# Kernel optimization log

Measured on AMD Instinct MI355X. Metric: run time of the kernel, lower is better.

## Reference

```python
import jax, jax.numpy as jnp
import numpy as np

NORM_EPS = 1e-5
HEAD_DIM = 32
SR_RATIO = 2
N_RATIO = SR_RATIO ** 2  # avg-pool kernel/stride over sequence


def setup_inputs() -> dict:
    key = jax.random.key(0)
    ks = jax.random.split(key, 12)
    B, N, C = 4, 3136, 384
    s = 0.02
    inp = {
        "x": jax.random.normal(ks[0], (B, N, C), dtype=jnp.float32),
        "Wq": jax.random.normal(ks[1], (C, C), dtype=jnp.float32) * s,
        "bq": jnp.zeros((C,), jnp.float32),
        "Wk": jax.random.normal(ks[2], (C, C), dtype=jnp.float32) * s,
        "bk": jnp.zeros((C,), jnp.float32),
        "Wv": jax.random.normal(ks[3], (C, C), dtype=jnp.float32) * s,
        "bv": jnp.zeros((C,), jnp.float32),
        "Wp": jax.random.normal(ks[4], (C, C), dtype=jnp.float32) * s,
        "bp": jnp.zeros((C,), jnp.float32),
        "bn_gamma": jnp.ones((C,), jnp.float32),
        "bn_beta": jnp.zeros((C,), jnp.float32),
        "bn_mean": jax.random.normal(ks[5], (C,), dtype=jnp.float32) * 0.1,
        "bn_var": jax.random.uniform(ks[6], (C,), dtype=jnp.float32, minval=0.5, maxval=1.5),
    }
    return inp


def reference(x, Wq, bq, Wk, bk, Wv, bv, Wp, bp, bn_gamma, bn_beta, bn_mean, bn_var):
    B, N, C = x.shape
    H = C // HEAD_DIM
    d = HEAD_DIM
    scale = d ** -0.5

    # q projection -> [B, H, N, d]
    q = (x @ Wq.T + bq).reshape(B, N, H, d)

    # sequence reduction: AvgPool1d(kernel=stride=N_RATIO) over tokens
    Nk = N // N_RATIO
    x_ = x.reshape(B, Nk, N_RATIO, C).mean(axis=2)  # [B, Nk, C]
    # BatchNorm1d over channel dim (inference / running-stats form)
    x_ = (x_ - bn_mean) * jax.lax.rsqrt(bn_var + NORM_EPS) * bn_gamma + bn_beta

    k = (x_ @ Wk.T + bk).reshape(B, Nk, H, d)
    v = (x_ @ Wv.T + bv).reshape(B, Nk, H, d)

    attn = jnp.einsum("bnhd,bmhd->bhnm", q, k) * scale  # [B, H, N, Nk]
    attn = jax.nn.softmax(attn, axis=-1)
    out = jnp.einsum("bhnm,bmhd->bnhd", attn, v).reshape(B, N, C)
    return out @ Wp.T + bp
```

## Files before the change

### kernel.cpp

```cpp
#include <hip/hip_runtime.h>


typedef __bf16 bf16x8 __attribute__((ext_vector_type(8)));
typedef unsigned short u16x8 __attribute__((ext_vector_type(8)));
typedef float f32x4 __attribute__((ext_vector_type(4)));

#define NTOK 3136
#define NKV 784
#define CCH 384
#define KPAD 832
#define SC2 0.25503472078024693f

#define WAIT_BAR(N) asm volatile("s_waitcnt vmcnt(" #N ")\n\ts_barrier" ::: "memory")

__device__ __forceinline__ unsigned short f2b(float f) {
  union { float f; unsigned u; } v; v.f = f;
  unsigned r = v.u + 0x7fffu + ((v.u >> 16) & 1u);
  return (unsigned short)(r >> 16);
}

__device__ __forceinline__ bf16x8 ldsb8(const unsigned short* p) {
  u16x8 v = *(const u16x8*)p;
  return __builtin_bit_cast(bf16x8, v);
}

__device__ __forceinline__ void gload16(const void* g, void* lds) {
  auto* g1 = reinterpret_cast<const __attribute__((address_space(1))) unsigned int*>(
      reinterpret_cast<uintptr_t>(g));
  auto* l3 = reinterpret_cast<__attribute__((address_space(3))) unsigned int*>(
      reinterpret_cast<uintptr_t>(lds));
  __builtin_amdgcn_global_load_lds(g1, l3, 16, 0, 0);
}

__global__ __launch_bounds__(256) void prep_kernel(
    const float* __restrict__ x, const float* __restrict__ gam,
    const float* __restrict__ bet, const float* __restrict__ mea,
    const float* __restrict__ var,
    const float* __restrict__ Wq, const float* __restrict__ Wk,
    const float* __restrict__ Wv, const float* __restrict__ Wp,
    unsigned short* __restrict__ xb, unsigned short* __restrict__ xpb,
    unsigned short* __restrict__ wq, unsigned short* __restrict__ wk,
    unsigned short* __restrict__ wv, unsigned short* __restrict__ wp,
    unsigned short* __restrict__ vt) {
  int bid = blockIdx.x;
  if (bid < 1176) {
    int i = bid * 256 + threadIdx.x;
    int c4 = i % 96;
    int row = i / 96;
    int b = row / NKV, nk = row - b * NKV;
    const float4* x4 = (const float4*)x;
    size_t base = ((size_t)(b * NTOK + nk * 4)) * 96 + c4;
    float sx = 0.f, sy = 0.f, sz = 0.f, sw = 0.f;
#pragma unroll
    for (int r = 0; r < 4; ++r) {
      float4 v = x4[base + (size_t)r * 96];
      ushort4 cv; cv.x = f2b(v.x); cv.y = f2b(v.y); cv.z = f2b(v.z); cv.w = f2b(v.w);
      ((ushort4*)xb)[base + (size_t)r * 96] = cv;
      sx += v.x; sy += v.y; sz += v.z; sw += v.w;
    }
    float4 g4 = ((const float4*)gam)[c4];
    float4 b4 = ((const float4*)bet)[c4];
    float4 m4 = ((const float4*)mea)[c4];
    float4 v4 = ((const float4*)var)[c4];
    ushort4 r4;
    r4.x = f2b((sx * 0.25f - m4.x) * rsqrtf(v4.x + 1e-5f) * g4.x + b4.x);
    r4.y = f2b((sy * 0.25f - m4.y) * rsqrtf(v4.y + 1e-5f) * g4.y + b4.y);
    r4.z = f2b((sz * 0.25f - m4.z) * rsqrtf(v4.z + 1e-5f) * g4.z + b4.z);
    r4.w = f2b((sw * 0.25f - m4.w) * rsqrtf(v4.w + 1e-5f) * g4.w + b4.w);
    ((ushort4*)xpb)[i] = r4;
  } else if (bid < 1320) {
    int i = (bid - 1176) * 256 + threadIdx.x;
    float4 va = ((const float4*)Wq)[i];
    float4 vb = ((const float4*)Wk)[i];
    float4 vc = ((const float4*)Wv)[i];
    float4 vd = ((const float4*)Wp)[i];
    ushort4 ra; ra.x = f2b(va.x); ra.y = f2b(va.y); ra.z = f2b(va.z); ra.w = f2b(va.w);
    ushort4 rb; rb.x = f2b(vb.x); rb.y = f2b(vb.y); rb.z = f2b(vb.z); rb.w = f2b(vb.w);
    ushort4 rc; rc.x = f2b(vc.x); rc.y = f2b(vc.y); rc.z = f2b(vc.z); rc.w = f2b(vc.w);
    ushort4 rd; rd.x = f2b(vd.x); rd.y = f2b(vd.y); rd.z = f2b(vd.z); rd.w = f2b(vd.w);
    ((ushort4*)wq)[i] = ra; ((ushort4*)wk)[i] = rb;
    ((ushort4*)wv)[i] = rc; ((ushort4*)wp)[i] = rd;
  } else {
    int i = (bid - 1320) * 256 + threadIdx.x;
    int row = i >> 4, quad = i & 15;
    ushort4 z; z.x = 0; z.y = 0; z.z = 0; z.w = 0;
    *(ushort4*)&vt[(size_t)row * KPAD + 768 + quad * 4] = z;
  }
}

template <int MR>
__device__ __forceinline__ void gemm_body(
    const unsigned short* __restrict__ A, const unsigned short* __restrict__ Bt,
    const float* __restrict__ bias, void* __restrict__ out,
    int row0, int col0, int epi, float oscale,
    unsigned short* sA, unsigned short* sB) {
  constexpr int ABUF = MR * 32;
  constexpr int MH = MR / 2;
  constexpr int NM = MR / 32;
  const int t = threadIdx.x, w = t >> 6, l = t & 63;
  const int wr = w >> 1, wc = w & 1;
  const int hi = l >> 4, c = l & 15;

  f32x4 acc[NM][4];
#pragma unroll
  for (int m = 0; m < NM; ++m)
#pragma unroll
    for (int n = 0; n < 4; ++n) acc[m][n] = (f32x4){0.f, 0.f, 0.f, 0.f};

  const unsigned short* Abase = A + (size_t)(row0 + l) * CCH + w * 8;
  const unsigned short* Abase2 = A + (size_t)(row0 + (MR == 128 ? 64 : 0) + l) * CCH + w * 8;
  const unsigned short* B0base = Bt + (size_t)(col0 + l) * CCH + w * 8;
  const unsigned short* B1base = Bt + (size_t)(col0 + 64 + l) * CCH + w * 8;

  auto STAGE = [&](int kk, int bsel) {
    if constexpr (MR == 128) {
      gload16(Abase + kk * 32, (char*)(sA + bsel * ABUF) + w * 2048);
      gload16(Abase2 + kk * 32, (char*)(sA + bsel * ABUF) + w * 2048 + 1024);
    } else {
      gload16(Abase + kk * 32, (char*)(sA + bsel * ABUF) + w * 1024);
    }
    gload16(B0base + kk * 32, (char*)(sB + bsel * 4096) + w * 2048);
    gload16(B1base + kk * 32, (char*)(sB + bsel * 4096) + w * 2048 + 1024);
  };

  STAGE(0, 0);
  STAGE(1, 1);
  if constexpr (MR == 128) WAIT_BAR(4); else WAIT_BAR(3);

#pragma unroll
  for (int kk = 0; kk < 12; ++kk) {
    const int cur = kk % 3;
    const int stg = (kk + 2) % 3;
    if (kk + 2 < 12) STAGE(kk + 2, stg);
    bf16x8 af[NM], bfv[4];
#pragma unroll
    for (int m = 0; m < NM; ++m)
      af[m] = ldsb8(sA + cur * ABUF + hi * (MR * 8) + (wr * MH + m * 16 + c) * 8);
#pragma unroll
    for (int n = 0; n < 4; ++n)
      bfv[n] = ldsb8(sB + cur * 4096 + hi * 1024 + (wc * 64 + n * 16 + c) * 8);
#pragma unroll
    for (int m = 0; m < NM; ++m)
#pragma unroll
      for (int n = 0; n < 4; ++n)
        acc[m][n] = __builtin_amdgcn_mfma_f32_16x16x32_bf16(af[m], bfv[n], acc[m][n], 0, 0, 0);
    if (kk + 1 < 12) {
      if (kk + 2 < 12) {
        if constexpr (MR == 128) WAIT_BAR(4); else WAIT_BAR(3);
      } else {
        WAIT_BAR(0);
      }
    }
  }

#pragma unroll
  for (int m = 0; m < NM; ++m) {
#pragma unroll
    for (int r = 0; r < 4; ++r) {
      int row = row0 + wr * MH + m * 16 + hi * 4 + r;
#pragma unroll
      for (int n = 0; n < 4; ++n) {
        int col = col0 + wc * 64 + n * 16 + c;
        float v = (acc[m][n][r] + bias[col]) * oscale;
        if (epi == 0) {
          ((unsigned short*)out)[(size_t)row * CCH + col] =
              __builtin_bit_cast(unsigned short, (__bf16)v);
        } else if (epi == 2) {
          ((float*)out)[(size_t)row * CCH + col] = v;
        } else {
          int b_ = row / NKV, j = row - b_ * NKV;
          int h_ = col >> 5, d = col & 31;
          int loc = j & 63;
          int kap = (j & ~63) + ((loc & 16) << 1) + ((loc & 12) << 1) +
                    ((loc & 32) >> 3) + (loc & 3);
          ((unsigned short*)out)[((size_t)((b_ * 12 + h_) * 32 + d)) * KPAD + kap] =
              __builtin_bit_cast(unsigned short, (__bf16)v);
        }
      }
    }
  }
}

__global__ __launch_bounds__(256) void qkv_kernel(
    const unsigned short* __restrict__ xb, const unsigned short* __restrict__ xpb,
    const unsigned short* __restrict__ wq, const unsigned short* __restrict__ wk,
    const unsigned short* __restrict__ wv,
    const float* __restrict__ bq, const float* __restrict__ bk,
    const float* __restrict__ bv,
    unsigned short* __restrict__ q_b, unsigned short* __restrict__ k_b,
    unsigned short* __restrict__ vt_b) {
  __shared__ unsigned short sA[3 * 4096];
  __shared__ unsigned short sB[3 * 4096];
  int bx = blockIdx.x, cy = blockIdx.y * 128;
  if (bx < 98) {
    gemm_body<128>(xb, wq, bq, (void*)q_b, bx * 128, cy, 0, SC2, sA, sB);
  } else if (bx < 147) {
    gemm_body<64>(xpb, wk, bk, (void*)k_b, (bx - 98) * 64, cy, 0, 1.f, sA, sB);
  } else {
    gemm_body<64>(xpb, wv, bv, (void*)vt_b, (bx - 147) * 64, cy, 1, 1.f, sA, sB);
  }
}

__global__ __launch_bounds__(256) void outproj_kernel(
    const unsigned short* __restrict__ ob, const unsigned short* __restrict__ wp,
    const float* __restrict__ bp_, float* __restrict__ out) {
  __shared__ unsigned short sA[3 * 4096];
  __shared__ unsigned short sB[3 * 4096];
  gemm_body<128>(ob, wp, bp_, (void*)out, blockIdx.x * 128, blockIdx.y * 128, 2, 1.f,
                 sA, sB);
}

__global__ __launch_bounds__(256) void attn_kernel(
    const unsigned short* __restrict__ qb, const unsigned short* __restrict__ kb,
    const unsigned short* __restrict__ vtb, unsigned short* __restrict__ ob) {
  __shared__ unsigned short sQ[4096];
  __shared__ unsigned short sK[3][2048];
  __shared__ unsigned short sV[3][2048];

  const int raw = blockIdx.x;
  const int lg = (raw & 7) * 150 + (raw >> 3);
  const int qt = lg % 25;
  const int h = (lg / 25) % 12;
  const int b = lg / 300;
  const int t = threadIdx.x, w = t >> 6, l = t & 63;
  const int q0 = qt * 128;
  const int hi = l >> 4, c = l & 15;

  const unsigned short* vbase = vtb + ((size_t)((b * 12 + h) * 32 + (l & 31))) * KPAD
                                + (2 * w + (l >> 5)) * 8;

  auto stageK = [&](int ttile, int bsel) {
    int j = ttile * 64 + l; if (j > NKV - 1) j = NKV - 1;
    gload16(kb + ((size_t)(b * NKV + j)) * CCH + h * 32 + w * 8,
            (char*)sK[bsel] + w * 1024);
  };
  auto stageV = [&](int ttile, int bsel) {
    gload16(vbase + ttile * 64, (char*)sV[bsel] + w * 1024);
  };

  {
    int r0 = q0 + l;            if (r0 > NTOK - 1) r0 = NTOK - 1;
    int r1 = q0 + 64 + l;       if (r1 > NTOK - 1) r1 = NTOK - 1;
    gload16(qb + ((size_t)(b * NTOK + r0)) * CCH + h * 32 + w * 8,
            (char*)sQ + w * 1024);
    gload16(qb + ((size_t)(b * NTOK + r1)) * CCH + h * 32 + w * 8,
            (char*)sQ + 4096 + w * 1024);
  }
  stageK(0, 0); stageV(0, 0);
  stageK(1, 1); stageV(1, 1);
  WAIT_BAR(2);

  const bf16x8 aq0 = ldsb8(&sQ[hi * 512 + (w * 16 + c) * 8]);
  const bf16x8 aq1 = ldsb8(&sQ[2048 + hi * 512 + (w * 16 + c) * 8]);
  bf16x8 ones;
#pragma unroll
  for (int i = 0; i < 8; ++i) ones[i] = (__bf16)1.0f;
  const f32x4 fz = (f32x4){0.f, 0.f, 0.f, 0.f};

  f32x4 a00 = fz, a01 = fz, al0 = fz;
  f32x4 a10 = fz, a11 = fz, al1 = fz;

#pragma unroll
  for (int tt = 0; tt < 13; ++tt) {
    const int cur = tt % 3;
    const int stg = (tt + 2) % 3;
    if (tt + 2 < 13) { stageK(tt + 2, stg); stageV(tt + 2, stg); }

    f32x4 s0[4], s1[4];
#pragma unroll
    for (int n = 0; n < 4; ++n) {
      bf16x8 kf = ldsb8(&sK[cur][hi * 512 + (n * 16 + c) * 8]);
      s0[n] = __builtin_amdgcn_mfma_f32_16x16x32_bf16(kf, aq0, fz, 0, 0, 0);
      s1[n] = __builtin_amdgcn_mfma_f32_16x16x32_bf16(kf, aq1, fz, 0, 0, 0);
    }

    bf16x8 pa00, pa01, pa10, pa11;
    {
      float p[4][4];
#pragma unroll
      for (int n = 0; n < 4; ++n)
#pragma unroll
        for (int r = 0; r < 4; ++r) p[n][r] = exp2f(s0[n][r]);
      if (tt == 12)
#pragma unroll
        for (int n = 1; n < 4; ++n)
#pragma unroll
          for (int r = 0; r < 4; ++r) p[n][r] = 0.f;
#pragma unroll
      for (int rr = 0; rr < 4; ++rr) {
        pa00[rr] = (__bf16)p[0][rr]; pa00[4 + rr] = (__bf16)p[2][rr];
        pa01[rr] = (__bf16)p[1][rr]; pa01[4 + rr] = (__bf16)p[3][rr];
      }
    }
    {
      float p[4][4];
#pragma unroll
      for (int n = 0; n < 4; ++n)
#pragma unroll
        for (int r = 0; r < 4; ++r) p[n][r] = exp2f(s1[n][r]);
      if (tt == 12)
#pragma unroll
        for (int n = 1; n < 4; ++n)
#pragma unroll
          for (int r = 0; r < 4; ++r) p[n][r] = 0.f;
#pragma unroll
      for (int rr = 0; rr < 4; ++rr) {
        pa10[rr] = (__bf16)p[0][rr]; pa10[4 + rr] = (__bf16)p[2][rr];
        pa11[rr] = (__bf16)p[1][rr]; pa11[4 + rr] = (__bf16)p[3][rr];
      }
    }

    __builtin_amdgcn_s_setprio(1);
#pragma unroll
    for (int kkk = 0; kkk < 2; ++kkk) {
      bf16x8 pg0 = kkk ? pa01 : pa00;
      bf16x8 pg1 = kkk ? pa11 : pa10;
      bf16x8 v0 = ldsb8(&sV[cur][(kkk * 4 + hi) * 256 + c * 8]);
      bf16x8 v1 = ldsb8(&sV[cur][(kkk * 4 + hi) * 256 + (16 + c) * 8]);
      a00 = __builtin_amdgcn_mfma_f32_16x16x32_bf16(pg0, v0, a00, 0, 0, 0);
      a10 = __builtin_amdgcn_mfma_f32_16x16x32_bf16(pg1, v0, a10, 0, 0, 0);
      a01 = __builtin_amdgcn_mfma_f32_16x16x32_bf16(pg0, v1, a01, 0, 0, 0);
      a11 = __builtin_amdgcn_mfma_f32_16x16x32_bf16(pg1, v1, a11, 0, 0, 0);
      al0 = __builtin_amdgcn_mfma_f32_16x16x32_bf16(pg0, ones, al0, 0, 0, 0);
      al1 = __builtin_amdgcn_mfma_f32_16x16x32_bf16(pg1, ones, al1, 0, 0, 0);
    }
    __builtin_amdgcn_s_setprio(0);

    if (tt + 1 < 13) {
      if (tt + 2 < 13) WAIT_BAR(2); else WAIT_BAR(0);
    }
  }

#pragma unroll
  for (int r = 0; r < 4; ++r) {
    int row = q0 + w * 16 + hi * 4 + r;
    float inv = 1.f / al0[r];
    size_t base = ((size_t)(b * NTOK + row)) * CCH + h * 32;
    ob[base + c] = __builtin_bit_cast(unsigned short, (__bf16)(a00[r] * inv));
    ob[base + 16 + c] = __builtin_bit_cast(unsigned short, (__bf16)(a01[r] * inv));
  }
#pragma unroll
  for (int r = 0; r < 4; ++r) {
    int row = q0 + 64 + w * 16 + hi * 4 + r;
    if (row < NTOK) {
      float inv = 1.f / al1[r];
      size_t base = ((size_t)(b * NTOK + row)) * CCH + h * 32;
      ob[base + c] = __builtin_bit_cast(unsigned short, (__bf16)(a10[r] * inv));
      ob[base + 16 + c] = __builtin_bit_cast(unsigned short, (__bf16)(a11[r] * inv));
    }
  }
}


extern "C" void kernel_launch(void* const* d_in, const int* in_sizes, int n_in,
                              void* d_out, int out_size, void* d_ws, size_t ws_size,
                              hipStream_t stream) {
  const float* x   = (const float*)d_in[0];
  const float* Wq  = (const float*)d_in[1];
  const float* bq  = (const float*)d_in[2];
  const float* Wk  = (const float*)d_in[3];
  const float* bk  = (const float*)d_in[4];
  const float* Wv  = (const float*)d_in[5];
  const float* bv  = (const float*)d_in[6];
  const float* Wp  = (const float*)d_in[7];
  const float* bp  = (const float*)d_in[8];
  const float* gam = (const float*)d_in[9];
  const float* bet = (const float*)d_in[10];
  const float* mea = (const float*)d_in[11];
  const float* var = (const float*)d_in[12];

  unsigned short* wq_b = (unsigned short*)d_ws;
  unsigned short* wk_b = wq_b + 147456;
  unsigned short* wv_b = wk_b + 147456;
  unsigned short* wp_b = wv_b + 147456;
  unsigned short* xb   = wp_b + 147456;
  unsigned short* x_b  = xb + 12544 * 384;
  unsigned short* q_b  = x_b + 3136 * 384;
  unsigned short* k_b  = q_b + 12544 * 384;
  unsigned short* vt_b = k_b + 3136 * 384;
  unsigned short* o_b  = vt_b + 1536 * KPAD;

  prep_kernel<<<1416, 256, 0, stream>>>(x, gam, bet, mea, var, Wq, Wk, Wv, Wp,
                                        xb, x_b, wq_b, wk_b, wv_b, wp_b, vt_b);
  qkv_kernel<<<dim3(196, 3), 256, 0, stream>>>(xb, x_b, wq_b, wk_b, wv_b,
                                               bq, bk, bv, q_b, k_b, vt_b);
  attn_kernel<<<1200, 256, 0, stream>>>(q_b, k_b, vt_b, o_b);
  outproj_kernel<<<dim3(98, 3), 256, 0, stream>>>(o_b, wp_b, bp, (float*)d_out);
}
```

Before: 92.62 us.

## Widen attention KV tiles to 128 with double buffering and raw v_exp

The attention kernel now processes 128 keys per iteration instead of 64, moving from a three-stage to a two-stage LDS pipeline. This halves the loop trips and barriers, with a special last tile covering the 16 leftover keys. The V-transpose layout is permuted for 128-key groups and padded to 896 columns, and prep launches more blocks to zero that larger padding. exp2f is replaced by inline v_exp_f32, and the setprio hints are dropped. The shallower pipeline with a full wait each iteration may expose more load latency.

```diff
diff --git a/kernel.cpp b/kernel.cpp
--- a/kernel.cpp
+++ b/kernel.cpp
@@ -8,7 +8,7 @@
 #define NTOK 3136
 #define NKV 784
 #define CCH 384
-#define KPAD 832
+#define KPAD 896
 #define SC2 0.25503472078024693f
 
 #define WAIT_BAR(N) asm volatile("s_waitcnt vmcnt(" #N ")\n\ts_barrier" ::: "memory")
@@ -82,7 +82,7 @@
     ((ushort4*)wv)[i] = rc; ((ushort4*)wp)[i] = rd;
   } else {
     int i = (bid - 1320) * 256 + threadIdx.x;
-    int row = i >> 4, quad = i & 15;
+    int row = i >> 5, quad = i & 31;
     ushort4 z; z.x = 0; z.y = 0; z.z = 0; z.w = 0;
     *(ushort4*)&vt[(size_t)row * KPAD + 768 + quad * 4] = z;
   }
@@ -170,9 +170,10 @@
         } else {
           int b_ = row / NKV, j = row - b_ * NKV;
           int h_ = col >> 5, d = col & 31;
-          int loc = j & 63;
-          int kap = (j & ~63) + ((loc & 16) << 1) + ((loc & 12) << 1) +
-                    ((loc & 32) >> 3) + (loc & 3);
+          int loc = j & 127;
+          int n_ = loc >> 4;
+          int kap = (j & ~127) + (n_ & 3) * 32 + ((loc >> 2) & 3) * 8 +
+                    (n_ >> 2) * 4 + (loc & 3);
           ((unsigned short*)out)[((size_t)((b_ * 12 + h_) * 32 + d)) * KPAD + kap] =
               __builtin_bit_cast(unsigned short, (__bf16)v);
         }
@@ -214,8 +215,8 @@
     const unsigned short* __restrict__ qb, const unsigned short* __restrict__ kb,
     const unsigned short* __restrict__ vtb, unsigned short* __restrict__ ob) {
   __shared__ unsigned short sQ[4096];
-  __shared__ unsigned short sK[3][2048];
-  __shared__ unsigned short sV[3][2048];
+  __shared__ unsigned short sK[2][4096];
+  __shared__ unsigned short sV[2][4096];
 
   const int raw = blockIdx.x;
   const int lg = (raw & 7) * 150 + (raw >> 3);
@@ -229,13 +230,16 @@
   const unsigned short* vbase = vtb + ((size_t)((b * 12 + h) * 32 + (l & 31))) * KPAD
                                 + (2 * w + (l >> 5)) * 8;
 
-  auto stageK = [&](int ttile, int bsel) {
-    int j = ttile * 64 + l; if (j > NKV - 1) j = NKV - 1;
-    gload16(kb + ((size_t)(b * NKV + j)) * CCH + h * 32 + w * 8,
-            (char*)sK[bsel] + w * 1024);
-  };
-  auto stageV = [&](int ttile, int bsel) {
-    gload16(vbase + ttile * 64, (char*)sV[bsel] + w * 1024);
+  auto stageKV = [&](int tt, int bsel) {
+    int j0 = tt * 128;
+    int ja = j0 + l;      if (ja > NKV - 1) ja = NKV - 1;
+    int jb = j0 + 64 + l; if (jb > NKV - 1) jb = NKV - 1;
+    gload16(kb + ((size_t)(b * NKV + ja)) * CCH + h * 32 + w * 8,
+            (char*)sK[bsel] + w * 2048);
+    gload16(kb + ((size_t)(b * NKV + jb)) * CCH + h * 32 + w * 8,
+            (char*)sK[bsel] + w * 2048 + 1024);
+    gload16(vbase + j0, (char*)sV[bsel] + w * 1024);
+    gload16(vbase + j0 + 64, (char*)sV[bsel] + 4096 + w * 1024);
   };
 
   {
@@ -246,9 +250,8 @@
     gload16(qb + ((size_t)(b * NTOK + r1)) * CCH + h * 32 + w * 8,
             (char*)sQ + 4096 + w * 1024);
   }
-  stageK(0, 0); stageV(0, 0);
-  stageK(1, 1); stageV(1, 1);
-  WAIT_BAR(2);
+  stageKV(0, 0);
+  WAIT_BAR(0);
 
   const bf16x8 aq0 = ldsb8(&sQ[hi * 512 + (w * 16 + c) * 8]);
   const bf16x8 aq1 = ldsb8(&sQ[2048 + hi * 512 + (w * 16 + c) * 8]);
@@ -261,74 +264,69 @@
   f32x4 a10 = fz, a11 = fz, al1 = fz;
 
 #pragma unroll
-  for (int tt = 0; tt < 13; ++tt) {
-    const int cur = tt % 3;
-    const int stg = (tt + 2) % 3;
-    if (tt + 2 < 13) { stageK(tt + 2, stg); stageV(tt + 2, stg); }
-
-    f32x4 s0[4], s1[4];
-#pragma unroll
-    for (int n = 0; n < 4; ++n) {
-      bf16x8 kf = ldsb8(&sK[cur][hi * 512 + (n * 16 + c) * 8]);
-      s0[n] = __builtin_amdgcn_mfma_f32_16x16x32_bf16(kf, aq0, fz, 0, 0, 0);
-      s1[n] = __builtin_amdgcn_mfma_f32_16x16x32_bf16(kf, aq1, fz, 0, 0, 0);
-    }
-
-    bf16x8 pa00, pa01, pa10, pa11;
-    {
-      float p[4][4];
-#pragma unroll
-      for (int n = 0; n < 4; ++n)
-#pragma unroll
-        for (int r = 0; r < 4; ++r) p[n][r] = exp2f(s0[n][r]);
-      if (tt == 12)
-#pragma unroll
-        for (int n = 1; n < 4; ++n)
-#pragma unroll
-          for (int r = 0; r < 4; ++r) p[n][r] = 0.f;
-#pragma unroll
-      for (int rr = 0; rr < 4; ++rr) {
-        pa00[rr] = (__bf16)p[0][rr]; pa00[4 + rr] = (__bf16)p[2][rr];
-        pa01[rr] = (__bf16)p[1][rr]; pa01[4 + rr] = (__bf16)p[3][rr];
-      }
-    }
-    {
-      float p[4][4];
-#pragma unroll
-      for (int n = 0; n < 4; ++n)
-#pragma unroll
-        for (int r = 0; r < 4; ++r) p[n][r] = exp2f(s1[n][r]);
-      if (tt == 12)
-#pragma unroll
-        for (int n = 1; n < 4; ++n)
-#pragma unroll
-          for (int r = 0; r < 4; ++r) p[n][r] = 0.f;
-#pragma unroll
-      for (int rr = 0; rr < 4; ++rr) {
-        pa10[rr] = (__bf16)p[0][rr]; pa10[4 + rr] = (__bf16)p[2][rr];
-        pa11[rr] = (__bf16)p[1][rr]; pa11[4 + rr] = (__bf16)p[3][rr];
-      }
-    }
-
-    __builtin_amdgcn_s_setprio(1);
-#pragma unroll
-    for (int kkk = 0; kkk < 2; ++kkk) {
-      bf16x8 pg0 = kkk ? pa01 : pa00;
-      bf16x8 pg1 = kkk ? pa11 : pa10;
-      bf16x8 v0 = ldsb8(&sV[cur][(kkk * 4 + hi) * 256 + c * 8]);
-      bf16x8 v1 = ldsb8(&sV[cur][(kkk * 4 + hi) * 256 + (16 + c) * 8]);
-      a00 = __builtin_amdgcn_mfma_f32_16x16x32_bf16(pg0, v0, a00, 0, 0, 0);
-      a10 = __builtin_amdgcn_mfma_f32_16x16x32_bf16(pg1, v0, a10, 0, 0, 0);
-      a01 = __builtin_amdgcn_mfma_f32_16x16x32_bf16(pg0, v1, a01, 0, 0, 0);
-      a11 = __builtin_amdgcn_mfma_f32_16x16x32_bf16(pg1, v1, a11, 0, 0, 0);
-      al0 = __builtin_amdgcn_mfma_f32_16x16x32_bf16(pg0, ones, al0, 0, 0, 0);
-      al1 = __builtin_amdgcn_mfma_f32_16x16x32_bf16(pg1, ones, al1, 0, 0, 0);
-    }
-    __builtin_amdgcn_s_setprio(0);
-
-    if (tt + 1 < 13) {
-      if (tt + 2 < 13) WAIT_BAR(2); else WAIT_BAR(0);
-    }
+  for (int tt = 0; tt < 7; ++tt) {
+    const int cur = tt & 1;
+    if (tt + 1 < 7) stageKV(tt + 1, cur ^ 1);
+
+    bf16x8 pa0[4], pa1[4];
+    if (tt < 6) {
+#pragma unroll
+      for (int kkk = 0; kkk < 4; ++kkk) {
+        bf16x8 kfa = ldsb8(&sK[cur][hi * 1024 + (kkk * 16 + c) * 8]);
+        bf16x8 kfb = ldsb8(&sK[cur][hi * 1024 + ((kkk + 4) * 16 + c) * 8]);
+        f32x4 sa0 = __builtin_amdgcn_mfma_f32_16x16x32_bf16(kfa, aq0, fz, 0, 0, 0);
+        f32x4 sb0 = __builtin_amdgcn_mfma_f32_16x16x32_bf16(kfb, aq0, fz, 0, 0, 0);
+        f32x4 sa1 = __builtin_amdgcn_mfma_f32_16x16x32_bf16(kfa, aq1, fz, 0, 0, 0);
+        f32x4 sb1 = __builtin_amdgcn_mfma_f32_16x16x32_bf16(kfb, aq1, fz, 0, 0, 0);
+#pragma unroll
+        for (int r = 0; r < 4; ++r) {
+          float e0, e1, e2, e3;
+          asm("v_exp_f32 %0, %1" : "=v"(e0) : "v"(sa0[r]));
+          asm("v_exp_f32 %0, %1" : "=v"(e1) : "v"(sb0[r]));
+          asm("v_exp_f32 %0, %1" : "=v"(e2) : "v"(sa1[r]));
+          asm("v_exp_f32 %0, %1" : "=v"(e3) : "v"(sb1[r]));
+          pa0[kkk][r] = (__bf16)e0; pa0[kkk][4 + r] = (__bf16)e1;
+          pa1[kkk][r] = (__bf16)e2; pa1[kkk][4 + r] = (__bf16)e3;
+        }
+      }
+    } else {
+      bf16x8 kfa = ldsb8(&sK[cur][hi * 1024 + c * 8]);
+      f32x4 sa0 = __builtin_amdgcn_mfma_f32_16x16x32_bf16(kfa, aq0, fz, 0, 0, 0);
+      f32x4 sa1 = __builtin_amdgcn_mfma_f32_16x16x32_bf16(kfa, aq1, fz, 0, 0, 0);
+#pragma unroll
+      for (int r = 0; r < 4; ++r) {
+        float e0, e2;
+        asm("v_exp_f32 %0, %1" : "=v"(e0) : "v"(sa0[r]));
+        asm("v_exp_f32 %0, %1" : "=v"(e2) : "v"(sa1[r]));
+        pa0[0][r] = (__bf16)e0; pa0[0][4 + r] = (__bf16)0.0f;
+        pa1[0][r] = (__bf16)e2; pa1[0][4 + r] = (__bf16)0.0f;
+      }
+    }
+
+    if (tt < 6) {
+#pragma unroll
+      for (int kkk = 0; kkk < 4; ++kkk) {
+        bf16x8 v0 = ldsb8(&sV[cur][(kkk * 4 + hi) * 256 + c * 8]);
+        bf16x8 v1 = ldsb8(&sV[cur][(kkk * 4 + hi) * 256 + (16 + c) * 8]);
+        a00 = __builtin_amdgcn_mfma_f32_16x16x32_bf16(pa0[kkk], v0, a00, 0, 0, 0);
+        a10 = __builtin_amdgcn_mfma_f32_16x16x32_bf16(pa1[kkk], v0, a10, 0, 0, 0);
+        a01 = __builtin_amdgcn_mfma_f32_16x16x32_bf16(pa0[kkk], v1, a01, 0, 0, 0);
+        a11 = __builtin_amdgcn_mfma_f32_16x16x32_bf16(pa1[kkk], v1, a11, 0, 0, 0);
+        al0 = __builtin_amdgcn_mfma_f32_16x16x32_bf16(pa0[kkk], ones, al0, 0, 0, 0);
+        al1 = __builtin_amdgcn_mfma_f32_16x16x32_bf16(pa1[kkk], ones, al1, 0, 0, 0);
+      }
+    } else {
+      bf16x8 v0 = ldsb8(&sV[cur][hi * 256 + c * 8]);
+      bf16x8 v1 = ldsb8(&sV[cur][hi * 256 + (16 + c) * 8]);
+      a00 = __builtin_amdgcn_mfma_f32_16x16x32_bf16(pa0[0], v0, a00, 0, 0, 0);
+      a10 = __builtin_amdgcn_mfma_f32_16x16x32_bf16(pa1[0], v0, a10, 0, 0, 0);
+      a01 = __builtin_amdgcn_mfma_f32_16x16x32_bf16(pa0[0], v1, a01, 0, 0, 0);
+      a11 = __builtin_amdgcn_mfma_f32_16x16x32_bf16(pa1[0], v1, a11, 0, 0, 0);
+      al0 = __builtin_amdgcn_mfma_f32_16x16x32_bf16(pa0[0], ones, al0, 0, 0, 0);
+      al1 = __builtin_amdgcn_mfma_f32_16x16x32_bf16(pa1[0], ones, al1, 0, 0, 0);
+    }
+
+    if (tt + 1 < 7) WAIT_BAR(0);
   }
 
 #pragma unroll
@@ -380,7 +378,7 @@
   unsigned short* vt_b = k_b + 3136 * 384;
   unsigned short* o_b  = vt_b + 1536 * KPAD;
 
-  prep_kernel<<<1416, 256, 0, stream>>>(x, gam, bet, mea, var, Wq, Wk, Wv, Wp,
+  prep_kernel<<<1512, 256, 0, stream>>>(x, gam, bet, mea, var, Wq, Wk, Wv, Wp,
                                         xb, x_b, wq_b, wk_b, wv_b, wp_b, vt_b);
   qkv_kernel<<<dim3(196, 3), 256, 0, stream>>>(xb, x_b, wq_b, wk_b, wv_b,
                                                bq, bk, bv, q_b, k_b, vt_b);
```

After: 79.01 us. -14.7%, faster.

## Double attention query tile to 256 rows per block to reuse K/V tiles

Applied to the files above, without the earlier changes.

Each attention block now processes 256 query rows (four 64-row groups) instead of 128, so every staged K/V tile in shared memory is reused across twice as many queries. The grid shrinks from 1200 to 624 blocks. K and V fragments are hoisted out of the per-group loop, and exp2f is replaced with raw v_exp_f32 inline asm. The cost is more accumulator registers and fewer blocks, which may reduce occupancy and latency hiding, and the last query tile is mostly padding.

```diff
diff --git a/kernel.cpp b/kernel.cpp
--- a/kernel.cpp
+++ b/kernel.cpp
@@ -213,17 +213,17 @@
 __global__ __launch_bounds__(256) void attn_kernel(
     const unsigned short* __restrict__ qb, const unsigned short* __restrict__ kb,
     const unsigned short* __restrict__ vtb, unsigned short* __restrict__ ob) {
-  __shared__ unsigned short sQ[4096];
+  __shared__ unsigned short sQ[8192];
   __shared__ unsigned short sK[3][2048];
   __shared__ unsigned short sV[3][2048];
 
   const int raw = blockIdx.x;
-  const int lg = (raw & 7) * 150 + (raw >> 3);
-  const int qt = lg % 25;
-  const int h = (lg / 25) % 12;
-  const int b = lg / 300;
+  const int lg = (raw & 7) * 78 + (raw >> 3);
+  const int qt = lg % 13;
+  const int h = (lg / 13) % 12;
+  const int b = lg / 156;
   const int t = threadIdx.x, w = t >> 6, l = t & 63;
-  const int q0 = qt * 128;
+  const int q0 = qt * 256;
   const int hi = l >> 4, c = l & 15;
 
   const unsigned short* vbase = vtb + ((size_t)((b * 12 + h) * 32 + (l & 31))) * KPAD
@@ -238,115 +238,100 @@
     gload16(vbase + ttile * 64, (char*)sV[bsel] + w * 1024);
   };
 
-  {
-    int r0 = q0 + l;            if (r0 > NTOK - 1) r0 = NTOK - 1;
-    int r1 = q0 + 64 + l;       if (r1 > NTOK - 1) r1 = NTOK - 1;
-    gload16(qb + ((size_t)(b * NTOK + r0)) * CCH + h * 32 + w * 8,
-            (char*)sQ + w * 1024);
-    gload16(qb + ((size_t)(b * NTOK + r1)) * CCH + h * 32 + w * 8,
-            (char*)sQ + 4096 + w * 1024);
+#pragma unroll
+  for (int g = 0; g < 4; ++g) {
+    int rq = q0 + g * 64 + l; if (rq > NTOK - 1) rq = NTOK - 1;
+    gload16(qb + ((size_t)(b * NTOK + rq)) * CCH + h * 32 + w * 8,
+            (char*)sQ + g * 4096 + w * 1024);
   }
   stageK(0, 0); stageV(0, 0);
   stageK(1, 1); stageV(1, 1);
-  WAIT_BAR(2);
-
-  const bf16x8 aq0 = ldsb8(&sQ[hi * 512 + (w * 16 + c) * 8]);
-  const bf16x8 aq1 = ldsb8(&sQ[2048 + hi * 512 + (w * 16 + c) * 8]);
+  WAIT_BAR(0);
+
+  bf16x8 aq[4];
+#pragma unroll
+  for (int g = 0; g < 4; ++g)
+    aq[g] = ldsb8(&sQ[g * 2048 + hi * 512 + (w * 16 + c) * 8]);
   bf16x8 ones;
 #pragma unroll
   for (int i = 0; i < 8; ++i) ones[i] = (__bf16)1.0f;
   const f32x4 fz = (f32x4){0.f, 0.f, 0.f, 0.f};
 
-  f32x4 a00 = fz, a01 = fz, al0 = fz;
-  f32x4 a10 = fz, a11 = fz, al1 = fz;
-
-#pragma unroll
+  f32x4 a0[4], a1[4], al[4];
+#pragma unroll
+  for (int g = 0; g < 4; ++g) { a0[g] = fz; a1[g] = fz; al[g] = fz; }
+
+  int cur = 0, stg = 2;
   for (int tt = 0; tt < 13; ++tt) {
-    const int cur = tt % 3;
-    const int stg = (tt + 2) % 3;
     if (tt + 2 < 13) { stageK(tt + 2, stg); stageV(tt + 2, stg); }
 
-    f32x4 s0[4], s1[4];
-#pragma unroll
-    for (int n = 0; n < 4; ++n) {
-      bf16x8 kf = ldsb8(&sK[cur][hi * 512 + (n * 16 + c) * 8]);
-      s0[n] = __builtin_amdgcn_mfma_f32_16x16x32_bf16(kf, aq0, fz, 0, 0, 0);
-      s1[n] = __builtin_amdgcn_mfma_f32_16x16x32_bf16(kf, aq1, fz, 0, 0, 0);
-    }
-
-    bf16x8 pa00, pa01, pa10, pa11;
-    {
+    bf16x8 kf[4], vf0[2], vf1[2];
+#pragma unroll
+    for (int n = 0; n < 4; ++n)
+      kf[n] = ldsb8(&sK[cur][hi * 512 + (n * 16 + c) * 8]);
+#pragma unroll
+    for (int kkk = 0; kkk < 2; ++kkk) {
+      vf0[kkk] = ldsb8(&sV[cur][(kkk * 4 + hi) * 256 + c * 8]);
+      vf1[kkk] = ldsb8(&sV[cur][(kkk * 4 + hi) * 256 + (16 + c) * 8]);
+    }
+
+    const bool tail = (tt == 12);
+#pragma unroll
+    for (int g = 0; g < 4; ++g) {
+      f32x4 s[4];
+#pragma unroll
+      for (int n = 0; n < 4; ++n)
+        s[n] = __builtin_amdgcn_mfma_f32_16x16x32_bf16(kf[n], aq[g], fz, 0, 0, 0);
+
       float p[4][4];
 #pragma unroll
       for (int n = 0; n < 4; ++n)
 #pragma unroll
-        for (int r = 0; r < 4; ++r) p[n][r] = exp2f(s0[n][r]);
-      if (tt == 12)
+        for (int r = 0; r < 4; ++r) {
+          float e;
+          asm("v_exp_f32 %0, %1" : "=v"(e) : "v"(s[n][r]));
+          p[n][r] = e;
+        }
+      if (tail)
 #pragma unroll
         for (int n = 1; n < 4; ++n)
 #pragma unroll
           for (int r = 0; r < 4; ++r) p[n][r] = 0.f;
+
+      bf16x8 pa0, pa1;
 #pragma unroll
       for (int rr = 0; rr < 4; ++rr) {
-        pa00[rr] = (__bf16)p[0][rr]; pa00[4 + rr] = (__bf16)p[2][rr];
-        pa01[rr] = (__bf16)p[1][rr]; pa01[4 + rr] = (__bf16)p[3][rr];
-      }
-    }
-    {
-      float p[4][4];
-#pragma unroll
-      for (int n = 0; n < 4; ++n)
-#pragma unroll
-        for (int r = 0; r < 4; ++r) p[n][r] = exp2f(s1[n][r]);
-      if (tt == 12)
-#pragma unroll
-        for (int n = 1; n < 4; ++n)
-#pragma unroll
-          for (int r = 0; r < 4; ++r) p[n][r] = 0.f;
-#pragma unroll
-      for (int rr = 0; rr < 4; ++rr) {
-        pa10[rr] = (__bf16)p[0][rr]; pa10[4 + rr] = (__bf16)p[2][rr];
-        pa11[rr] = (__bf16)p[1][rr]; pa11[4 + rr] = (__bf16)p[3][rr];
-      }
-    }
-
-    __builtin_amdgcn_s_setprio(1);
-#pragma unroll
-    for (int kkk = 0; kkk < 2; ++kkk) {
-      bf16x8 pg0 = kkk ? pa01 : pa00;
-      bf16x8 pg1 = kkk ? pa11 : pa10;
-      bf16x8 v0 = ldsb8(&sV[cur][(kkk * 4 + hi) * 256 + c * 8]);
-      bf16x8 v1 = ldsb8(&sV[cur][(kkk * 4 + hi) * 256 + (16 + c) * 8]);
-      a00 = __builtin_amdgcn_mfma_f32_16x16x32_bf16(pg0, v0, a00, 0, 0, 0);
-      a10 = __builtin_amdgcn_mfma_f32_16x16x32_bf16(pg1, v0, a10, 0, 0, 0);
-      a01 = __builtin_amdgcn_mfma_f32_16x16x32_bf16(pg0, v1, a01, 0, 0, 0);
-      a11 = __builtin_amdgcn_mfma_f32_16x16x32_bf16(pg1, v1, a11, 0, 0, 0);
-      al0 = __builtin_amdgcn_mfma_f32_16x16x32_bf16(pg0, ones, al0, 0, 0, 0);
-      al1 = __builtin_amdgcn_mfma_f32_16x16x32_bf16(pg1, ones, al1, 0, 0, 0);
-    }
-    __builtin_amdgcn_s_setprio(0);
+        pa0[rr] = (__bf16)p[0][rr]; pa0[4 + rr] = (__bf16)p[2][rr];
+        pa1[rr] = (__bf16)p[1][rr]; pa1[4 + rr] = (__bf16)p[3][rr];
+      }
+
+#pragma unroll
+      for (int kkk = 0; kkk < 2; ++kkk) {
+        bf16x8 pg = kkk ? pa1 : pa0;
+        a0[g] = __builtin_amdgcn_mfma_f32_16x16x32_bf16(pg, vf0[kkk], a0[g], 0, 0, 0);
+        a1[g] = __builtin_amdgcn_mfma_f32_16x16x32_bf16(pg, vf1[kkk], a1[g], 0, 0, 0);
+        al[g] = __builtin_amdgcn_mfma_f32_16x16x32_bf16(pg, ones, al[g], 0, 0, 0);
+      }
+    }
 
     if (tt + 1 < 13) {
       if (tt + 2 < 13) WAIT_BAR(2); else WAIT_BAR(0);
     }
-  }
-
-#pragma unroll
-  for (int r = 0; r < 4; ++r) {
-    int row = q0 + w * 16 + hi * 4 + r;
-    float inv = 1.f / al0[r];
-    size_t base = ((size_t)(b * NTOK + row)) * CCH + h * 32;
-    ob[base + c] = __builtin_bit_cast(unsigned short, (__bf16)(a00[r] * inv));
-    ob[base + 16 + c] = __builtin_bit_cast(unsigned short, (__bf16)(a01[r] * inv));
-  }
-#pragma unroll
-  for (int r = 0; r < 4; ++r) {
-    int row = q0 + 64 + w * 16 + hi * 4 + r;
-    if (row < NTOK) {
-      float inv = 1.f / al1[r];
-      size_t base = ((size_t)(b * NTOK + row)) * CCH + h * 32;
-      ob[base + c] = __builtin_bit_cast(unsigned short, (__bf16)(a10[r] * inv));
-      ob[base + 16 + c] = __builtin_bit_cast(unsigned short, (__bf16)(a11[r] * inv));
+    cur = (cur == 2) ? 0 : cur + 1;
+    stg = (stg == 2) ? 0 : stg + 1;
+  }
+
+#pragma unroll
+  for (int g = 0; g < 4; ++g) {
+#pragma unroll
+    for (int r = 0; r < 4; ++r) {
+      int row = q0 + g * 64 + w * 16 + hi * 4 + r;
+      if (row < NTOK) {
+        float inv = 1.f / al[g][r];
+        size_t base = ((size_t)(b * NTOK + row)) * CCH + h * 32;
+        ob[base + c] = __builtin_bit_cast(unsigned short, (__bf16)(a0[g][r] * inv));
+        ob[base + 16 + c] = __builtin_bit_cast(unsigned short, (__bf16)(a1[g][r] * inv));
+      }
     }
   }
 }
@@ -384,6 +369,6 @@
                                         xb, x_b, wq_b, wk_b, wv_b, wp_b, vt_b);
   qkv_kernel<<<dim3(196, 3), 256, 0, stream>>>(xb, x_b, wq_b, wk_b, wv_b,
                                                bq, bk, bv, q_b, k_b, vt_b);
-  attn_kernel<<<1200, 256, 0, stream>>>(q_b, k_b, vt_b, o_b);
+  attn_kernel<<<624, 256, 0, stream>>>(q_b, k_b, vt_b, o_b);
   outproj_kernel<<<dim3(98, 3), 256, 0, stream>>>(o_b, wp_b, bp, (float*)d_out);
 }
```

Result: faster. 89.90 us (-2.9%).
